# Kernel tuning notes

Measured on AMD Instinct MI355X. Metric: run time of the kernel, lower is better.

## Reference

```python
import jax, jax.numpy as jnp
import numpy as np

NUM_HEADS = 8
DIM = 192  # target_dim = min(channels_list)
CHANNELS = [192, 384, 768]
SIZES = [(32, 32), (16, 16), (8, 8)]
BATCH = 4


def conv1x1(x, w, b):
    # x: [B,C,H,W], w: [O,C,1,1], b: [O]
    y = jnp.einsum('bchw,oc->bohw', x, w[:, :, 0, 0])
    return y + b[None, :, None, None]


def cross_attention(x, ctx, wq, wkv, wp, bp):
    # x: [B,N,C] queries, ctx: [B,M,C] key/value source
    B, N, C = x.shape
    M = ctx.shape[1]
    h = NUM_HEADS
    d = C // h
    scale = d ** -0.5
    q = (x @ wq.T).reshape(B, N, h, d).transpose(0, 2, 1, 3)          # [B,h,N,d]
    kv = ctx @ wkv.T                                                   # [B,M,2C]
    k = kv[..., :C].reshape(B, M, h, d).transpose(0, 2, 1, 3)          # [B,h,M,d]
    v = kv[..., C:].reshape(B, M, h, d).transpose(0, 2, 1, 3)          # [B,h,M,d]
    attn = jax.nn.softmax(jnp.einsum('bhnd,bhmd->bhnm', q, k) * scale, axis=-1)
    o = jnp.einsum('bhnm,bhmd->bhnd', attn, v)
    o = o.transpose(0, 2, 1, 3).reshape(B, N, C)
    return o @ wp.T + bp


def setup_inputs() -> dict:
    key = jax.random.key(0)
    ks = iter(jax.random.split(key, 64))
    s = 0.02
    inp = {}
    for i, (c, (H, W)) in enumerate(zip(CHANNELS, SIZES)):
        inp[f'f{i}'] = jax.random.normal(next(ks), (BATCH, c, H, W), dtype=jnp.float32)
    # input projections (scale 0 has c == target_dim -> Identity, no params)
    for i in (1, 2):
        c = CHANNELS[i]
        inp[f'proj{i}_w'] = jax.random.normal(next(ks), (DIM, c, 1, 1), dtype=jnp.float32) * s
        inp[f'proj{i}_b'] = jnp.zeros((DIM,), dtype=jnp.float32)
    # cross-attention params per scale (qkv_bias=False; proj has bias)
    for i in range(3):
        inp[f'q{i}_w'] = jax.random.normal(next(ks), (DIM, DIM), dtype=jnp.float32) * s
        inp[f'kv{i}_w'] = jax.random.normal(next(ks), (2 * DIM, DIM), dtype=jnp.float32) * s
        inp[f'pr{i}_w'] = jax.random.normal(next(ks), (DIM, DIM), dtype=jnp.float32) * s
        inp[f'pr{i}_b'] = jnp.zeros((DIM,), dtype=jnp.float32)
    # output projections back to each channel count
    for i, c in enumerate(CHANNELS):
        inp[f'out{i}_w'] = jax.random.normal(next(ks), (c, DIM, 1, 1), dtype=jnp.float32) * s
        inp[f'out{i}_b'] = jnp.zeros((c,), dtype=jnp.float32)
    return inp


def _forward(f0, f1, f2,
             proj1_w, proj1_b, proj2_w, proj2_b,
             q0_w, kv0_w, pr0_w, pr0_b,
             q1_w, kv1_w, pr1_w, pr1_b,
             q2_w, kv2_w, pr2_w, pr2_b,
             out0_w, out0_b, out1_w, out1_b, out2_w, out2_b):
    projected = [
        f0,  # Identity (channels == target_dim)
        conv1x1(f1, proj1_w, proj1_b),
        conv1x1(f2, proj2_w, proj2_b),
    ]
    attn_params = [
        (q0_w, kv0_w, pr0_w, pr0_b),
        (q1_w, kv1_w, pr1_w, pr1_b),
        (q2_w, kv2_w, pr2_w, pr2_b),
    ]
    out_params = [(out0_w, out0_b), (out1_w, out1_b), (out2_w, out2_b)]
    outputs = []
    for i in range(3):
        feat = projected[i]
        B, C, H, W = feat.shape
        x = feat.reshape(B, C, H * W).transpose(0, 2, 1)  # [B,N,C]
        ctxs = []
        for j in range(3):
            if j != i:
                r = jax.image.resize(projected[j], (B, C, H, W), method='bilinear', antialias=False)
                ctxs.append(r.reshape(B, C, H * W).transpose(0, 2, 1))
        ctx = jnp.concatenate(ctxs, axis=1)  # [B,M,C]
        enh = cross_attention(x, ctx, *attn_params[i])
        enh = enh.transpose(0, 2, 1).reshape(B, C, H, W) + feat
        outputs.append(conv1x1(enh, *out_params[i]))
    return tuple(outputs)


def reference(f0, f1, f2,
              proj1_w, proj1_b, proj2_w, proj2_b,
              q0_w, kv0_w, pr0_w, pr0_b,
              q1_w, kv1_w, pr1_w, pr1_b,
              q2_w, kv2_w, pr2_w, pr2_b,
              out0_w, out0_b, out1_w, out1_b, out2_w, out2_b):
    return _forward(f0, f1, f2,
                    proj1_w, proj1_b, proj2_w, proj2_b,
                    q0_w, kv0_w, pr0_w, pr0_b,
                    q1_w, kv1_w, pr1_w, pr1_b,
                    q2_w, kv2_w, pr2_w, pr2_b,
                    out0_w, out0_b, out1_w, out1_b, out2_w, out2_b)
```

## Files before the change

kernel.cpp:

```cpp
#include <hip/hip_runtime.h>
#include <math.h>

#define BB 4
#define DIM 192
#define HEADS 8
#define HD 24

typedef __attribute__((ext_vector_type(8))) short short8v;
typedef __attribute__((ext_vector_type(4))) short short4v;
typedef __attribute__((ext_vector_type(4))) float f32x4;
typedef __attribute__((ext_vector_type(4))) unsigned uint4v;

__device__ __forceinline__ short f2bf(float f) {
  unsigned u = __builtin_bit_cast(unsigned, f);
  u += 0x7FFF + ((u >> 16) & 1);
  return (short)(u >> 16);
}
__device__ __forceinline__ unsigned pk2(float a, float b) {
  return (unsigned)(unsigned short)f2bf(a) | ((unsigned)(unsigned short)f2bf(b) << 16);
}
__device__ __forceinline__ float bf2f(unsigned u16) {
  return __builtin_bit_cast(float, u16 << 16);
}
__device__ __forceinline__ void gl_lds16(const void* g, void* l) {
  __builtin_amdgcn_global_load_lds(
      (const __attribute__((address_space(1))) unsigned int*)g,
      (__attribute__((address_space(3))) unsigned int*)l, 16, 0, 0);
}
__device__ __forceinline__ int xcd_swz(int bid, int nwg) {
  int q = nwg >> 3, r = nwg & 7;
  int xcd = bid & 7, idx = bid >> 3;
  return (xcd < r) ? (xcd * (q + 1) + idx) : (r * (q + 1) + (xcd - r) * q + idx);
}

struct PJob {
  int type;
  const float* s0; const float* s1; const float* s2;
  void* dst;
  int P0, P1v;
  int t_begin, t_end;
};
struct PJobs { PJob j[20]; };

__global__ __launch_bounds__(256) void prep_k(PJobs jobs, int nj) {
  int tid = blockIdx.x * 256 + threadIdx.x;
  for (int ji = 0; ji < 20; ++ji) {
    if (ji >= nj) return;
    PJob g = jobs.j[ji];
    if (tid < g.t_begin || tid >= g.t_end) continue;
    int t = tid - g.t_begin;
    if (g.type == 0) {
      float4 v = *(const float4*)&g.s0[(size_t)t * 4];
      uint2 u = {pk2(v.x, v.y), pk2(v.z, v.w)};
      *(uint2*)&((short*)g.dst)[(size_t)t * 4] = u;
    } else if (g.type == 1) {
      int X = g.P0, C = g.P1v, C8 = C >> 3;
      int x = t % X, c8 = (t / X) % C8, b = t / (X * C8);
      const float* s = g.s0 + ((size_t)b * C + c8 * 8) * X + x;
      unsigned h[8];
#pragma unroll
      for (int j = 0; j < 8; ++j) h[j] = (unsigned)(unsigned short)f2bf(s[(size_t)j * X]);
      uint4 u = {h[0] | (h[1] << 16), h[2] | (h[3] << 16), h[4] | (h[5] << 16), h[6] | (h[7] << 16)};
      *(uint4*)&((short*)g.dst)[((size_t)b * X + x) * C + c8 * 8] = u;
    } else if (g.type == 2) {
      int o = t;
      const float* w = g.s0 + (size_t)o * 192;
      float acc = g.s2[o];
      for (int k = 0; k < 192; ++k) acc += w[k] * g.s1[k];
      ((float*)g.dst)[o] = acc;
    } else {
      int c4 = t % 48, o = t / 48;
      const float* w = g.s0 + (size_t)o * 192;
      float a0 = 0, a1 = 0, a2 = 0, a3 = 0;
      for (int k = 0; k < 192; ++k) {
        float wv = w[k];
        float4 pv = *(const float4*)&g.s1[(size_t)k * 192 + c4 * 4];
        a0 += wv * pv.x; a1 += wv * pv.y; a2 += wv * pv.z; a3 += wv * pv.w;
      }
      uint2 u = {pk2(a0, a1), pk2(a2, a3)};
      *(uint2*)&((short*)g.dst)[(size_t)o * 192 + c4 * 4] = u;
    }
    return;
  }
}

struct MJob {
  const short* A; const short* W; const float* bias; const float* T;
  void* out;
  int K, nOT, mode, tokPerB;
  float scale;
  int blk_begin, blk_end;
};
struct MJobs { MJob j[10]; };

__global__ __launch_bounds__(256) void mgemm_k(MJobs jobs, int nj, int nwg) {
  __shared__ short Asl[64 * 192];
  __shared__ short Wsl[64 * 192];
  int blk = xcd_swz(blockIdx.x, nwg);
  for (int ji = 0; ji < 10; ++ji) {
    if (ji >= nj) return;
    MJob g = jobs.j[ji];
    if (blk < g.blk_begin || blk >= g.blk_end) continue;
    int lb = blk - g.blk_begin;
    int ot = lb % g.nOT, tt = lb / g.nOT;
    int t0 = tt * 64, o0 = ot * 64;
    int tid = threadIdx.x, wv = tid >> 6, lane = tid & 63, c = lane & 15, qi = lane >> 4;
    const int K = g.K;
    int rowK[6];
#pragma unroll
    for (int i = 0; i < 6; ++i) {
      int o16 = i * 256 + tid;
      int row = o16 / 24, ch = o16 - row * 24;
      rowK[i] = row * K + ((ch ^ (row & 7)) << 3);
    }
    const short* Ab = g.A + (size_t)t0 * K;
    const short* Wb = g.W + (size_t)o0 * K;
    f32x4 acc[4];
#pragma unroll
    for (int jj = 0; jj < 4; ++jj) acc[jj] = (f32x4){0.f, 0.f, 0.f, 0.f};
    int nkc = K / 192;
    int swz = c & 7;
    for (int kc = 0; kc < nkc; ++kc) {
      if (kc) __syncthreads();
      int kco = kc * 192;
#pragma unroll
      for (int i = 0; i < 6; ++i) gl_lds16(Ab + rowK[i] + kco, &Asl[(i * 256 + wv * 64) * 8]);
#pragma unroll
      for (int i = 0; i < 6; ++i) gl_lds16(Wb + rowK[i] + kco, &Wsl[(i * 256 + wv * 64) * 8]);
      asm volatile("s_waitcnt vmcnt(0)" ::: "memory");
      __syncthreads();
      const short* Lb = (g.mode == 0) ? Wsl : Asl;
      const short* Rb = (g.mode == 0) ? Asl : Wsl;
      int lrow = wv * 16 + c;
#pragma unroll
      for (int ks = 0; ks < 6; ++ks) {
        int chx = ((ks * 4 + qi) ^ swz) << 3;
        short8v lf = *(const short8v*)&Lb[lrow * 192 + chx];
#pragma unroll
        for (int jj = 0; jj < 4; ++jj) {
          short8v rf = *(const short8v*)&Rb[(jj * 16 + c) * 192 + chx];
          acc[jj] = __builtin_amdgcn_mfma_f32_16x16x32_bf16(lf, rf, acc[jj], 0, 0, 0);
        }
      }
    }
    int OST = g.nOT * 64;
    if (g.mode == 0) {
      int ob = o0 + wv * 16 + (qi << 2);
      float4 bv = {0.f, 0.f, 0.f, 0.f};
      if (g.bias) bv = *(const float4*)&g.bias[ob];
      float s = g.scale;
      short* op = (short*)g.out;
#pragma unroll
      for (int jj = 0; jj < 4; ++jj) {
        size_t tok = t0 + jj * 16 + c;
        uint2 u = {pk2(acc[jj][0] * s + bv.x, acc[jj][1] * s + bv.y),
                   pk2(acc[jj][2] * s + bv.z, acc[jj][3] * s + bv.w)};
        *(uint2*)&op[tok * OST + ob] = u;
      }
    } else {
      int tokb = t0 + wv * 16;
      int b = tokb / g.tokPerB;
      int nl = tokb - b * g.tokPerB + (qi << 2);
#pragma unroll
      for (int jj = 0; jj < 4; ++jj) {
        int o = o0 + jj * 16 + c;
        size_t idx = ((size_t)b * OST + o) * g.tokPerB + nl;
        if (g.mode == 1) {
          uint2 u = {pk2(acc[jj][0], acc[jj][1]), pk2(acc[jj][2], acc[jj][3])};
          *(uint2*)&((short*)g.out)[idx] = u;
        } else if (g.mode == 2) {
          float4 tv = *(const float4*)&g.T[idx];
          float4 ov = {acc[jj][0] + tv.x, acc[jj][1] + tv.y, acc[jj][2] + tv.z, acc[jj][3] + tv.w};
          *(float4*)&((float*)g.out)[idx] = ov;
        } else {
          float bvv = g.bias ? g.bias[o] : 0.f;
          float4 ov = {acc[jj][0] + bvv, acc[jj][1] + bvv, acc[jj][2] + bvv, acc[jj][3] + bvv};
          *(float4*)&((float*)g.out)[idx] = ov;
        }
      }
    }
    return;
  }
}

struct RJob {
  const short* src;
  short* dst;
  int Hs, Ws, Wd, Mtot;
  float ry, rx;
  int t_begin, t_end;
};
struct RJobs { RJob j[6]; };

__global__ __launch_bounds__(256) void resize_k(RJobs jobs) {
  int tid = blockIdx.x * 256 + threadIdx.x;
  for (int ji = 0; ji < 6; ++ji) {
    RJob g = jobs.j[ji];
    if (tid < g.t_begin || tid >= g.t_end) continue;
    int t = tid - g.t_begin;
    int c8 = t % 24;
    int rest = t / 24;
    int HWd = g.Wd * g.Wd;
    int n = rest % HWd, b = rest / HWd;
    int y = n / g.Wd, x = n % g.Wd;
    float fy = (y + 0.5f) * g.ry - 0.5f;
    float fx = (x + 0.5f) * g.rx - 0.5f;
    int y0 = (int)floorf(fy), x0 = (int)floorf(fx);
    float wy = fy - (float)y0, wx = fx - (float)x0;
    int Hs = g.Hs, Ws = g.Ws;
    int y0c = min(max(y0, 0), Hs - 1), y1c = min(max(y0 + 1, 0), Hs - 1);
    int x0c = min(max(x0, 0), Ws - 1), x1c = min(max(x0 + 1, 0), Ws - 1);
    size_t sb = (size_t)b * Hs * Ws;
    const short* sp = g.src;
    uint4 u00 = *(const uint4*)&sp[(sb + y0c * Ws + x0c) * 192 + c8 * 8];
    uint4 u01 = *(const uint4*)&sp[(sb + y0c * Ws + x1c) * 192 + c8 * 8];
    uint4 u10 = *(const uint4*)&sp[(sb + y1c * Ws + x0c) * 192 + c8 * 8];
    uint4 u11 = *(const uint4*)&sp[(sb + y1c * Ws + x1c) * 192 + c8 * 8];
    float w00 = (1.f - wy) * (1.f - wx), w01 = (1.f - wy) * wx;
    float w10 = wy * (1.f - wx), w11 = wy * wx;
    unsigned a[4], bq[4], cq[4], dq[4];
    a[0]=u00.x; a[1]=u00.y; a[2]=u00.z; a[3]=u00.w;
    bq[0]=u01.x; bq[1]=u01.y; bq[2]=u01.z; bq[3]=u01.w;
    cq[0]=u10.x; cq[1]=u10.y; cq[2]=u10.z; cq[3]=u10.w;
    dq[0]=u11.x; dq[1]=u11.y; dq[2]=u11.z; dq[3]=u11.w;
    unsigned r[4];
#pragma unroll
    for (int k = 0; k < 4; ++k) {
      float lo = w00 * bf2f(a[k] & 0xffff) + w01 * bf2f(bq[k] & 0xffff) +
                 w10 * bf2f(cq[k] & 0xffff) + w11 * bf2f(dq[k] & 0xffff);
      float hi = w00 * bf2f(a[k] >> 16) + w01 * bf2f(bq[k] >> 16) +
                 w10 * bf2f(cq[k] >> 16) + w11 * bf2f(dq[k] >> 16);
      r[k] = pk2(lo, hi);
    }
    uint4 u = {r[0], r[1], r[2], r[3]};
    *(uint4*)&g.dst[((size_t)b * g.Mtot + n) * 192 + c8 * 8] = u;
    return;
  }
}

struct AJob {
  const short* q;
  const short* K;
  const short* V;
  short* o;
  int N, M;
  int blk_begin, blk_end;
};
struct AJobs { AJob j[3]; };

__global__ __launch_bounds__(256) void attn_k(AJobs jobs, int cpx) {
  __shared__ __align__(16) short LDSbuf[2][7432];
  int bid = blockIdx.x;
  int blk = (bid & 7) * cpx + (bid >> 3);
  int tidx = threadIdx.x;
  if (tidx < 4) {
    ((int*)LDSbuf[0])[1536 + tidx] = 0;
    ((int*)LDSbuf[1])[1536 + tidx] = 0;
  }
  if (tidx < 64) {
    ((int*)LDSbuf[0])[3172 + tidx] = 0x3F803F80;
    ((int*)LDSbuf[1])[3172 + tidx] = 0x3F803F80;
  }
  for (int ji = 0; ji < 3; ++ji) {
    AJob g = jobs.j[ji];
    if (blk < g.blk_begin || blk >= g.blk_end) continue;
    int lb = blk - g.blk_begin;
    const int N = g.N, M = g.M;
    int nch = N >> 6;
    int bh = lb / nch, ct = lb % nch;
    int b = bh >> 3, h = bh & 7;
    int wv = tidx >> 6, lane = tidx & 63;
    int c = lane & 15, qi = lane >> 4;
    int nw0 = (ct << 6) + (wv << 4);

    const short* Kg = g.K + (size_t)b * M * 192 + h * 24;
    const short* Vg = g.V + ((size_t)b * 192 + h * 24) * M;

    const short* gp[4];
    int gstr[4], loff[4];
    bool val[4];
#pragma unroll
    for (int i = 0; i < 4; ++i) {
      int s = tidx + (i << 8);
      val[i] = (s < 792);
      if (s < 384) {
        int row = s / 3, part = s - row * 3;
        gp[i] = Kg + row * 192 + part * 8;
        gstr[i] = 128 * 192;
        loff[i] = s * 8;
      } else {
        int v = s - 384;
        int row = v / 17, col = v - row * 17;
        int colc = (col < 16) ? col : 0;
        gp[i] = val[i] ? (Vg + (size_t)row * M + colc * 8) : Vg;
        gstr[i] = 128;
        loff[i] = 3080 + v * 8;
      }
    }

    short8v qf = *(const short8v*)&g.q[((size_t)b * N + nw0 + c) * 192 + h * 24 + (qi << 3)];
    if (qi == 3) {
#pragma unroll
      for (int j = 0; j < 8; ++j) qf[j] = 0;
    }

    f32x4 of0 = {0.f, 0.f, 0.f, 0.f}, of1 = {0.f, 0.f, 0.f, 0.f};
    const f32x4 zf = {0.f, 0.f, 0.f, 0.f};

#pragma unroll
    for (int i = 0; i < 4; ++i)
      if (val[i]) { gl_lds16(gp[i], &LDSbuf[0][loff[i]]); gp[i] += gstr[i]; }

    int nt = M >> 7;
    int cur = 0;
    for (int t = 0; t < nt; ++t) {
      asm volatile("s_waitcnt vmcnt(0)" ::: "memory");
      __syncthreads();
      if (t + 1 < nt) {
#pragma unroll
        for (int i = 0; i < 4; ++i)
          if (val[i]) { gl_lds16(gp[i], &LDSbuf[cur ^ 1][loff[i]]); gp[i] += gstr[i]; }
      }
      const short* Kl = LDSbuf[cur];
      const short* Vl = LDSbuf[cur] + 3080;
      f32x4 sr[8];
#pragma unroll
      for (int jj = 0; jj < 8; ++jj) {
        short8v kb = *(const short8v*)&Kl[(c + 16 * jj) * 24 + (qi << 3)];
        sr[jj] = __builtin_amdgcn_mfma_f32_16x16x32_bf16(kb, qf, zf, 0, 0, 0);
      }
      unsigned pk[8][2];
#pragma unroll
      for (int jj = 0; jj < 8; ++jj) {
        pk[jj][0] = pk2(__expf(sr[jj][0]), __expf(sr[jj][1]));
        pk[jj][1] = pk2(__expf(sr[jj][2]), __expf(sr[jj][3]));
      }
#pragma unroll
      for (int ks = 0; ks < 4; ++ks) {
        uint4v pu = {pk[2 * ks][0], pk[2 * ks][1], pk[2 * ks + 1][0], pk[2 * ks + 1][1]};
        short8v pa = __builtin_bit_cast(short8v, pu);
        int vb0 = c * 136 + ks * 32 + (qi << 2);
        int vb1 = (16 + c) * 136 + ks * 32 + (qi << 2);
        short4v l0 = *(const short4v*)&Vl[vb0];
        short4v h0 = *(const short4v*)&Vl[vb0 + 16];
        short4v l1 = *(const short4v*)&Vl[vb1];
        short4v h1 = *(const short4v*)&Vl[vb1 + 16];
        short8v v0, v1;
#pragma unroll
        for (int j2 = 0; j2 < 4; ++j2) {
          v0[j2] = l0[j2]; v0[4 + j2] = h0[j2];
          v1[j2] = l1[j2]; v1[4 + j2] = h1[j2];
        }
        of0 = __builtin_amdgcn_mfma_f32_16x16x32_bf16(pa, v0, of0, 0, 0, 0);
        of1 = __builtin_amdgcn_mfma_f32_16x16x32_bf16(pa, v1, of1, 0, 0, 0);
      }
      cur ^= 1;
    }
    float ls[4];
#pragma unroll
    for (int r = 0; r < 4; ++r) ls[r] = __shfl(of1[r], (qi << 4) + 8);
#pragma unroll
    for (int r = 0; r < 4; ++r) {
      float inv = 1.f / ls[r];
      int n = nw0 + (qi << 2) + r;
      short* op = g.o + ((size_t)b * N + n) * 192 + h * 24;
      op[c] = f2bf(of0[r] * inv);
      if (c < 8) op[16 + c] = f2bf(of1[r] * inv);
    }
    return;
  }
}

extern "C" void kernel_launch(void* const* d_in, const int* in_sizes, int n_in,
                              void* d_out, int out_size, void* d_ws, size_t ws_size,
                              hipStream_t stream) {
  (void)in_sizes; (void)n_in; (void)out_size; (void)ws_size;
  const float* f0 = (const float*)d_in[0];
  const float* f1 = (const float*)d_in[1];
  const float* f2 = (const float*)d_in[2];
  const float* p1w = (const float*)d_in[3];
  const float* p1b = (const float*)d_in[4];
  const float* p2w = (const float*)d_in[5];
  const float* p2b = (const float*)d_in[6];
  const float* qw[3]  = {(const float*)d_in[7],  (const float*)d_in[11], (const float*)d_in[15]};
  const float* kvw[3] = {(const float*)d_in[8],  (const float*)d_in[12], (const float*)d_in[16]};
  const float* prw[3] = {(const float*)d_in[9],  (const float*)d_in[13], (const float*)d_in[17]};
  const float* prb[3] = {(const float*)d_in[10], (const float*)d_in[14], (const float*)d_in[18]};
  const float* ow[3]  = {(const float*)d_in[19], (const float*)d_in[21], (const float*)d_in[23]};
  const float* ob[3]  = {(const float*)d_in[20], (const float*)d_in[22], (const float*)d_in[24]};

  char* ws = (char*)d_ws;
  short* x0    = (short*)(ws + 0);
  short* x1in  = (short*)(ws + 1572864);
  short* x2in  = (short*)(ws + 2359296);
  short* P1    = (short*)(ws + 2752512);
  short* P2    = (short*)(ws + 3145728);
  short* ctx0  = (short*)(ws + 3244032);
  short* ctx1  = (short*)(ws + 6389760);
  short* ctx2  = (short*)(ws + 7176192);
  short* qb    = (short*)(ws + 7372800);
  short* Kb    = (short*)(ws + 9437184);
  short* Vb    = (short*)(ws + 13565952);
  short* attb  = (short*)(ws + 17694720);
  float* T0    = (float*)(ws + 19759104);
  float* T1    = (float*)(ws + 22904832);
  float* T2    = (float*)(ws + 24477696);
  short* W2b   = (short*)(ws + 25264128);
  short* wcvt  = (short*)(ws + 25780224);
  float* bfin  = (float*)(ws + 27402240);

  short* p1w_b = wcvt;
  short* p2w_b = wcvt + 73728;
  short* qw_b[3]  = {wcvt + 221184, wcvt + 258048, wcvt + 294912};
  short* kvw_b[3] = {wcvt + 331776, wcvt + 405504, wcvt + 479232};
  short* ow_b[3]  = {wcvt + 552960, wcvt + 589824, wcvt + 663552};
  short* W2_b[3]  = {W2b, W2b + 36864, W2b + 110592};
  short* qs[3]  = {qb, qb + 786432, qb + 983040};
  short* Ks[3]  = {Kb, Kb + 1572864, Kb + 1966080};
  short* Vs[3]  = {Vb, Vb + 1572864, Vb + 1966080};
  short* atts[3] = {attb, attb + 786432, attb + 983040};
  float* out0 = (float*)d_out;
  float* outp[3] = {out0, out0 + 786432, out0 + 1179648};

  const int Ns[3] = {1024, 256, 64};
  const int Ms[3] = {2048, 512, 128};
  const float qsc = 0.20412414523193154f;

  {
    PJobs js{};
    int t0 = 0, n = 0;
    auto add = [&](PJob j, int tc) { j.t_begin = t0; j.t_end = t0 + tc; js.j[n++] = j; t0 += tc; };
    add({0, p1w, nullptr, nullptr, p1w_b, 0, 0, 0, 0}, 18432);
    add({0, p2w, nullptr, nullptr, p2w_b, 0, 0, 0, 0}, 36864);
    for (int i = 0; i < 3; ++i) add({0, qw[i], nullptr, nullptr, qw_b[i], 0, 0, 0, 0}, 9216);
    for (int i = 0; i < 3; ++i) add({0, kvw[i], nullptr, nullptr, kvw_b[i], 0, 0, 0, 0}, 18432);
    add({0, ow[0], nullptr, nullptr, ow_b[0], 0, 0, 0, 0}, 9216);
    add({0, ow[1], nullptr, nullptr, ow_b[1], 0, 0, 0, 0}, 18432);
    add({0, ow[2], nullptr, nullptr, ow_b[2], 0, 0, 0, 0}, 36864);
    add({1, f0, nullptr, nullptr, x0, 1024, 192, 0, 0}, 98304);
    add({1, f1, nullptr, nullptr, x1in, 256, 384, 0, 0}, 49152);
    add({1, f2, nullptr, nullptr, x2in, 64, 768, 0, 0}, 24576);
    add({2, ow[0], prb[0], ob[0], bfin, 0, 0, 0, 0}, 192);
    add({2, ow[1], prb[1], ob[1], bfin + 192, 0, 0, 0, 0}, 384);
    add({2, ow[2], prb[2], ob[2], bfin + 576, 0, 0, 0, 0}, 768);
    add({3, ow[0], prw[0], nullptr, W2_b[0], 0, 0, 0, 0}, 9216);
    add({3, ow[1], prw[1], nullptr, W2_b[1], 0, 0, 0, 0}, 18432);
    add({3, ow[2], prw[2], nullptr, W2_b[2], 0, 0, 0, 0}, 36864);
    hipLaunchKernelGGL(prep_k, dim3((t0 + 255) / 256), dim3(256), 0, stream, js, n);
  }
  {
    MJobs js{};
    int b0 = 0, n = 0;
    auto add = [&](MJob j, int nb) { j.blk_begin = b0; j.blk_end = b0 + nb; js.j[n++] = j; b0 += nb; };
    add({x1in, p1w_b, p1b, nullptr, P1, 384, 3, 0, 0, 1.f, 0, 0}, 16 * 3);
    add({x2in, p2w_b, p2b, nullptr, P2, 768, 3, 0, 0, 1.f, 0, 0}, 4 * 3);
    add({x0, qw_b[0], nullptr, nullptr, qs[0], 192, 3, 0, 0, qsc, 0, 0}, 64 * 3);
    add({x0, ow_b[0], bfin, nullptr, T0, 192, 3, 3, 1024, 1.f, 0, 0}, 64 * 3);
    hipLaunchKernelGGL(mgemm_k, dim3(b0), dim3(256), 0, stream, js, n, b0);
  }
  {
    RJobs js{};
    int t0 = 0, n = 0;
    auto add = [&](RJob j, int tc) { j.t_begin = t0; j.t_end = t0 + tc; js.j[n++] = j; t0 += tc; };
    add({P1, ctx0, 16, 16, 32, 2048, 0.5f, 0.5f, 0, 0}, 98304);
    add({P2, ctx0 + 1024 * 192, 8, 8, 32, 2048, 0.25f, 0.25f, 0, 0}, 98304);
    add({x0, ctx1, 32, 32, 16, 512, 2.f, 2.f, 0, 0}, 24576);
    add({P2, ctx1 + 256 * 192, 8, 8, 16, 512, 0.5f, 0.5f, 0, 0}, 24576);
    add({x0, ctx2, 32, 32, 8, 128, 4.f, 4.f, 0, 0}, 6144);
    add({P1, ctx2 + 64 * 192, 16, 16, 8, 128, 2.f, 2.f, 0, 0}, 6144);
    hipLaunchKernelGGL(resize_k, dim3(t0 / 256), dim3(256), 0, stream, js);
  }
  {
    MJobs js{};
    int b0 = 0, n = 0;
    auto add = [&](MJob j, int nb) { j.blk_begin = b0; j.blk_end = b0 + nb; js.j[n++] = j; b0 += nb; };
    add({P1, qw_b[1], nullptr, nullptr, qs[1], 192, 3, 0, 0, qsc, 0, 0}, 16 * 3);
    add({P2, qw_b[2], nullptr, nullptr, qs[2], 192, 3, 0, 0, qsc, 0, 0}, 4 * 3);
    add({ctx0, kvw_b[0], nullptr, nullptr, Ks[0], 192, 3, 0, 0, 1.f, 0, 0}, 128 * 3);
    add({ctx1, kvw_b[1], nullptr, nullptr, Ks[1], 192, 3, 0, 0, 1.f, 0, 0}, 32 * 3);
    add({ctx2, kvw_b[2], nullptr, nullptr, Ks[2], 192, 3, 0, 0, 1.f, 0, 0}, 8 * 3);
    add({ctx0, kvw_b[0] + 36864, nullptr, nullptr, Vs[0], 192, 3, 1, 2048, 1.f, 0, 0}, 128 * 3);
    add({ctx1, kvw_b[1] + 36864, nullptr, nullptr, Vs[1], 192, 3, 1, 512, 1.f, 0, 0}, 32 * 3);
    add({ctx2, kvw_b[2] + 36864, nullptr, nullptr, Vs[2], 192, 3, 1, 128, 1.f, 0, 0}, 8 * 3);
    add({P1, ow_b[1], bfin + 192, nullptr, T1, 192, 6, 3, 256, 1.f, 0, 0}, 16 * 6);
    add({P2, ow_b[2], bfin + 576, nullptr, T2, 192, 12, 3, 64, 1.f, 0, 0}, 4 * 12);
    hipLaunchKernelGGL(mgemm_k, dim3(b0), dim3(256), 0, stream, js, n, b0);
  }
  {
    AJobs js{};
    int b0 = 0;
    for (int i = 0; i < 3; ++i) {
      int nb = BB * HEADS * (Ns[i] / 64);
      js.j[i] = {qs[i], Ks[i], Vs[i], atts[i], Ns[i], Ms[i], b0, b0 + nb};
      b0 += nb;
    }
    hipLaunchKernelGGL(attn_k, dim3(b0), dim3(256), 0, stream, js, b0 / 8);
  }
  {
    MJobs js{};
    int b0 = 0, n = 0;
    auto add = [&](MJob j, int nb) { j.blk_begin = b0; j.blk_end = b0 + nb; js.j[n++] = j; b0 += nb; };
    add({atts[0], W2_b[0], nullptr, T0, outp[0], 192, 3, 2, 1024, 1.f, 0, 0}, 64 * 3);
    add({atts[1], W2_b[1], nullptr, T1, outp[1], 192, 6, 2, 256, 1.f, 0, 0}, 16 * 6);
    add({atts[2], W2_b[2], nullptr, T2, outp[2], 192, 12, 2, 64, 1.f, 0, 0}, 4 * 12);
    hipLaunchKernelGGL(mgemm_k, dim3(b0), dim3(256), 0, stream, js, n, b0);
  }
}
```

Baseline: 89.52 us.

## Process 128 queries per attention block and move weight fold to MFMA GEMM

Each attention wave now handles two 16-query tiles against the same K/V LDS tile, so each block covers 128 queries. This halves K/V global-to-LDS traffic and block count, and reuses K/V fragments across two MFMA chains. Separately, the scalar fp32 out_w·proj_w weight fold in the prep kernel is replaced by transposing proj_w to bf16 and running the fold as extra jobs in the first MFMA GEMM launch. The cost is more registers per wave and fewer attention blocks, which may reduce occupancy and parallelism for the small N=64 scale.

```diff
diff --git a/kernel.cpp b/kernel.cpp
--- a/kernel.cpp
+++ b/kernel.cpp
@@ -62,23 +62,12 @@
       for (int j = 0; j < 8; ++j) h[j] = (unsigned)(unsigned short)f2bf(s[(size_t)j * X]);
       uint4 u = {h[0] | (h[1] << 16), h[2] | (h[3] << 16), h[4] | (h[5] << 16), h[6] | (h[7] << 16)};
       *(uint4*)&((short*)g.dst)[((size_t)b * X + x) * C + c8 * 8] = u;
-    } else if (g.type == 2) {
+    } else {
       int o = t;
       const float* w = g.s0 + (size_t)o * 192;
       float acc = g.s2[o];
       for (int k = 0; k < 192; ++k) acc += w[k] * g.s1[k];
       ((float*)g.dst)[o] = acc;
-    } else {
-      int c4 = t % 48, o = t / 48;
-      const float* w = g.s0 + (size_t)o * 192;
-      float a0 = 0, a1 = 0, a2 = 0, a3 = 0;
-      for (int k = 0; k < 192; ++k) {
-        float wv = w[k];
-        float4 pv = *(const float4*)&g.s1[(size_t)k * 192 + c4 * 4];
-        a0 += wv * pv.x; a1 += wv * pv.y; a2 += wv * pv.z; a3 += wv * pv.w;
-      }
-      uint2 u = {pk2(a0, a1), pk2(a2, a3)};
-      *(uint2*)&((short*)g.dst)[(size_t)o * 192 + c4 * 4] = u;
     }
     return;
   }
@@ -266,12 +255,12 @@
     if (blk < g.blk_begin || blk >= g.blk_end) continue;
     int lb = blk - g.blk_begin;
     const int N = g.N, M = g.M;
-    int nch = N >> 6;
+    int nch = N >> 7; if (!nch) nch = 1;
     int bh = lb / nch, ct = lb % nch;
     int b = bh >> 3, h = bh & 7;
     int wv = tidx >> 6, lane = tidx & 63;
     int c = lane & 15, qi = lane >> 4;
-    int nw0 = (ct << 6) + (wv << 4);
+    int nw0 = (ct << 7) + (wv << 5);
 
     const short* Kg = g.K + (size_t)b * M * 192 + h * 24;
     const short* Vg = g.V + ((size_t)b * 192 + h * 24) * M;
@@ -298,13 +287,17 @@
       }
     }
 
-    short8v qf = *(const short8v*)&g.q[((size_t)b * N + nw0 + c) * 192 + h * 24 + (qi << 3)];
+    int r1 = (nw0 + c) & (N - 1);
+    int r2 = (nw0 + 16 + c) & (N - 1);
+    short8v qf1 = *(const short8v*)&g.q[((size_t)b * N + r1) * 192 + h * 24 + (qi << 3)];
+    short8v qf2 = *(const short8v*)&g.q[((size_t)b * N + r2) * 192 + h * 24 + (qi << 3)];
     if (qi == 3) {
 #pragma unroll
-      for (int j = 0; j < 8; ++j) qf[j] = 0;
+      for (int j = 0; j < 8; ++j) { qf1[j] = 0; qf2[j] = 0; }
     }
 
     f32x4 of0 = {0.f, 0.f, 0.f, 0.f}, of1 = {0.f, 0.f, 0.f, 0.f};
+    f32x4 of2 = {0.f, 0.f, 0.f, 0.f}, of3 = {0.f, 0.f, 0.f, 0.f};
     const f32x4 zf = {0.f, 0.f, 0.f, 0.f};
 
 #pragma unroll
@@ -323,22 +316,23 @@
       }
       const short* Kl = LDSbuf[cur];
       const short* Vl = LDSbuf[cur] + 3080;
-      f32x4 sr[8];
+      unsigned pka[8][2], pkb[8][2];
 #pragma unroll
       for (int jj = 0; jj < 8; ++jj) {
         short8v kb = *(const short8v*)&Kl[(c + 16 * jj) * 24 + (qi << 3)];
-        sr[jj] = __builtin_amdgcn_mfma_f32_16x16x32_bf16(kb, qf, zf, 0, 0, 0);
-      }
-      unsigned pk[8][2];
-#pragma unroll
-      for (int jj = 0; jj < 8; ++jj) {
-        pk[jj][0] = pk2(__expf(sr[jj][0]), __expf(sr[jj][1]));
-        pk[jj][1] = pk2(__expf(sr[jj][2]), __expf(sr[jj][3]));
+        f32x4 s1 = __builtin_amdgcn_mfma_f32_16x16x32_bf16(kb, qf1, zf, 0, 0, 0);
+        f32x4 s2 = __builtin_amdgcn_mfma_f32_16x16x32_bf16(kb, qf2, zf, 0, 0, 0);
+        pka[jj][0] = pk2(__expf(s1[0]), __expf(s1[1]));
+        pka[jj][1] = pk2(__expf(s1[2]), __expf(s1[3]));
+        pkb[jj][0] = pk2(__expf(s2[0]), __expf(s2[1]));
+        pkb[jj][1] = pk2(__expf(s2[2]), __expf(s2[3]));
       }
 #pragma unroll
       for (int ks = 0; ks < 4; ++ks) {
-        uint4v pu = {pk[2 * ks][0], pk[2 * ks][1], pk[2 * ks + 1][0], pk[2 * ks + 1][1]};
-        short8v pa = __builtin_bit_cast(short8v, pu);
+        uint4v pu1 = {pka[2 * ks][0], pka[2 * ks][1], pka[2 * ks + 1][0], pka[2 * ks + 1][1]};
+        uint4v pu2 = {pkb[2 * ks][0], pkb[2 * ks][1], pkb[2 * ks + 1][0], pkb[2 * ks + 1][1]};
+        short8v pa1 = __builtin_bit_cast(short8v, pu1);
+        short8v pa2 = __builtin_bit_cast(short8v, pu2);
         int vb0 = c * 136 + ks * 32 + (qi << 2);
         int vb1 = (16 + c) * 136 + ks * 32 + (qi << 2);
         short4v l0 = *(const short4v*)&Vl[vb0];
@@ -351,21 +345,33 @@
           v0[j2] = l0[j2]; v0[4 + j2] = h0[j2];
           v1[j2] = l1[j2]; v1[4 + j2] = h1[j2];
         }
-        of0 = __builtin_amdgcn_mfma_f32_16x16x32_bf16(pa, v0, of0, 0, 0, 0);
-        of1 = __builtin_amdgcn_mfma_f32_16x16x32_bf16(pa, v1, of1, 0, 0, 0);
+        of0 = __builtin_amdgcn_mfma_f32_16x16x32_bf16(pa1, v0, of0, 0, 0, 0);
+        of1 = __builtin_amdgcn_mfma_f32_16x16x32_bf16(pa1, v1, of1, 0, 0, 0);
+        of2 = __builtin_amdgcn_mfma_f32_16x16x32_bf16(pa2, v0, of2, 0, 0, 0);
+        of3 = __builtin_amdgcn_mfma_f32_16x16x32_bf16(pa2, v1, of3, 0, 0, 0);
       }
       cur ^= 1;
     }
-    float ls[4];
-#pragma unroll
-    for (int r = 0; r < 4; ++r) ls[r] = __shfl(of1[r], (qi << 4) + 8);
+    float ls1[4], ls2[4];
 #pragma unroll
     for (int r = 0; r < 4; ++r) {
-      float inv = 1.f / ls[r];
-      int n = nw0 + (qi << 2) + r;
-      short* op = g.o + ((size_t)b * N + n) * 192 + h * 24;
-      op[c] = f2bf(of0[r] * inv);
-      if (c < 8) op[16 + c] = f2bf(of1[r] * inv);
+      ls1[r] = __shfl(of1[r], (qi << 4) + 8);
+      ls2[r] = __shfl(of3[r], (qi << 4) + 8);
+    }
+    if (nw0 < N) {
+#pragma unroll
+      for (int r = 0; r < 4; ++r) {
+        float inv1 = 1.f / ls1[r];
+        int n1 = nw0 + (qi << 2) + r;
+        short* op1 = g.o + ((size_t)b * N + n1) * 192 + h * 24;
+        op1[c] = f2bf(of0[r] * inv1);
+        if (c < 8) op1[16 + c] = f2bf(of1[r] * inv1);
+        float inv2 = 1.f / ls2[r];
+        int n2 = nw0 + 16 + (qi << 2) + r;
+        short* op2 = g.o + ((size_t)b * N + n2) * 192 + h * 24;
+        op2[c] = f2bf(of2[r] * inv2);
+        if (c < 8) op2[16 + c] = f2bf(of3[r] * inv2);
+      }
     }
     return;
   }
@@ -408,12 +414,14 @@
   short* W2b   = (short*)(ws + 25264128);
   short* wcvt  = (short*)(ws + 25780224);
   float* bfin  = (float*)(ws + 27402240);
+  short* prwT  = (short*)(ws + 27407616);
 
   short* p1w_b = wcvt;
   short* p2w_b = wcvt + 73728;
   short* qw_b[3]  = {wcvt + 221184, wcvt + 258048, wcvt + 294912};
   short* kvw_b[3] = {wcvt + 331776, wcvt + 405504, wcvt + 479232};
   short* ow_b[3]  = {wcvt + 552960, wcvt + 589824, wcvt + 663552};
+  short* prwT_b[3] = {prwT, prwT + 36864, prwT + 73728};
   short* W2_b[3]  = {W2b, W2b + 36864, W2b + 110592};
   short* qs[3]  = {qb, qb + 786432, qb + 983040};
   short* Ks[3]  = {Kb, Kb + 1572864, Kb + 1966080};
@@ -424,6 +432,7 @@
 
   const int Ns[3] = {1024, 256, 64};
   const int Ms[3] = {2048, 512, 128};
+  const int Couts[3] = {192, 384, 768};
   const float qsc = 0.20412414523193154f;
 
   {
@@ -440,12 +449,11 @@
     add({1, f0, nullptr, nullptr, x0, 1024, 192, 0, 0}, 98304);
     add({1, f1, nullptr, nullptr, x1in, 256, 384, 0, 0}, 49152);
     add({1, f2, nullptr, nullptr, x2in, 64, 768, 0, 0}, 24576);
+    for (int i = 0; i < 3; ++i)
+      add({1, prw[i], nullptr, nullptr, prwT_b[i], 192, 192, 0, 0}, 4608);
     add({2, ow[0], prb[0], ob[0], bfin, 0, 0, 0, 0}, 192);
     add({2, ow[1], prb[1], ob[1], bfin + 192, 0, 0, 0, 0}, 384);
     add({2, ow[2], prb[2], ob[2], bfin + 576, 0, 0, 0, 0}, 768);
-    add({3, ow[0], prw[0], nullptr, W2_b[0], 0, 0, 0, 0}, 9216);
-    add({3, ow[1], prw[1], nullptr, W2_b[1], 0, 0, 0, 0}, 18432);
-    add({3, ow[2], prw[2], nullptr, W2_b[2], 0, 0, 0, 0}, 36864);
     hipLaunchKernelGGL(prep_k, dim3((t0 + 255) / 256), dim3(256), 0, stream, js, n);
   }
   {
@@ -456,6 +464,9 @@
     add({x2in, p2w_b, p2b, nullptr, P2, 768, 3, 0, 0, 1.f, 0, 0}, 4 * 3);
     add({x0, qw_b[0], nullptr, nullptr, qs[0], 192, 3, 0, 0, qsc, 0, 0}, 64 * 3);
     add({x0, ow_b[0], bfin, nullptr, T0, 192, 3, 3, 1024, 1.f, 0, 0}, 64 * 3);
+    for (int i = 0; i < 3; ++i)
+      add({ow_b[i], prwT_b[i], nullptr, nullptr, W2_b[i], 192, 3, 0, 0, 1.f, 0, 0},
+          (Couts[i] / 64) * 3);
     hipLaunchKernelGGL(mgemm_k, dim3(b0), dim3(256), 0, stream, js, n, b0);
   }
   {
@@ -490,7 +501,8 @@
     AJobs js{};
     int b0 = 0;
     for (int i = 0; i < 3; ++i) {
-      int nb = BB * HEADS * (Ns[i] / 64);
+      int nchunks = Ns[i] >= 128 ? Ns[i] / 128 : 1;
+      int nb = BB * HEADS * nchunks;
       js.j[i] = {qs[i], Ks[i], Vs[i], atts[i], Ns[i], Ms[i], b0, b0 + nb};
       b0 += nb;
     }
```

After: 91.81 us. 1.03x slower.
